# Optimization experiments

Measured on AMD Instinct MI355X. Metric: run time of the kernel, lower is better.

The kernel has to match this reference:

```python
import jax, jax.numpy as jnp
import numpy as np

INV_SQRT2 = 0.7071067811865476


def _quadrature_ops(d):
    # truncated harmonic-oscillator ladder operator: a[n, n+1] = sqrt(n+1)
    a = jnp.diag(jnp.sqrt(jnp.arange(1, d, dtype=jnp.float32)), k=1)
    X0 = (a + a.T) * INV_SQRT2
    P0 = (a - a.T) * INV_SQRT2  # real-valued stand-in for the momentum quadrature
    I = jnp.eye(d, dtype=jnp.float32)
    return I, X0, P0


def setup_inputs() -> dict:
    key = jax.random.key(0)
    ks = jax.random.split(key, 6)
    D, d, w, K = 512, 32, 8, 4
    return {
        "mps_params": jax.random.normal(ks[0], (D, d, D), dtype=jnp.float32),
        "theta": jax.random.normal(ks[1], (1,), dtype=jnp.float32),
        "env_L": jax.random.normal(ks[2], (K, D, w, D), dtype=jnp.float32) * 0.1,
        "env_R": jax.random.normal(ks[3], (K, D, w, D), dtype=jnp.float32) * 0.1,
        "coeffs": jax.random.normal(ks[4], (K, w, w, 5), dtype=jnp.float32),
        "prefactors": jax.random.normal(ks[5], (K,), dtype=jnp.float32),
    }


def reference(mps_params, theta, env_L, env_R, coeffs, prefactors):
    A = mps_params  # [D(left), d(phys), D(right)]
    d = A.shape[1]
    K = prefactors.shape[0]

    # norm_fn: psi.H @ psi for a single-tensor MPS is sum(A^2)
    An = A / jnp.sqrt(jnp.sum(A * A))

    # _get_XandP: quadrature rotation from basis params
    I, X0, P0 = _quadrature_ops(d)
    c, s = jnp.cos(theta[0]), jnp.sin(theta[0])
    X = c * X0 + s * P0
    P = -s * X0 + c * P0

    # dynamic MPO cores: W_k[i,j] = sum_c coeffs[k,i,j,c] * ops[c]
    ops = jnp.stack([I, X, P, X @ X, P @ P])  # [5, d, d]
    W = jnp.einsum('kijc,cab->kijab', coeffs, ops)  # [K, w, w, d, d]

    out = jnp.zeros((), dtype=A.dtype)
    for k in range(K):  # fixed small loop over Hamiltonian constituents
        # T: [L, w, p, r]
        T = jnp.einsum('Lwl,lpr->Lwpr', env_L[k], An)
        # apply MPO core: [L, v, P, r]
        T = jnp.einsum('wvPp,Lwpr->LvPr', W[k], T)
        # close with right env: [L, P, R]
        T = jnp.einsum('LvPr,Rvr->LPR', T, env_R[k])
        out = out + prefactors[k] * jnp.einsum('LPR,LPR->', An, T)
    return out
```

## Files before the change

kernel.cpp:

```cpp
#include <hip/hip_runtime.h>


typedef __attribute__((ext_vector_type(8))) _Float16 f16x8;
typedef __attribute__((ext_vector_type(4))) float f32x4;

#define EPS 136

__device__ __forceinline__ unsigned short f2h(float f) {
    _Float16 h = (_Float16)f;
    return *(unsigned short*)&h;
}

__device__ __forceinline__ void gload16(const void* g, void* l) {
    __builtin_amdgcn_global_load_lds(
        (const __attribute__((address_space(1))) void*)g,
        (__attribute__((address_space(3))) void*)l, 16, 0, 0);
}

struct GArg {
    const unsigned short* A;
    const unsigned short* B;
    unsigned short* C;
    int kshift;
    long long kextra;
};

__global__ __launch_bounds__(256) void gemm_dual(int K, GArg g0, GArg g1)
{
    __shared__ short sh[8704];
    const GArg g = blockIdx.z ? g1 : g0;
    const int tid = threadIdx.x;
    const int wid = tid >> 6, lane = tid & 63;

    const int flat = blockIdx.y * 128 + blockIdx.x;
    const int xcd = flat & 7;
    const int local = flat >> 3;
    const int col0 = (xcd * 16 + (local & 15)) * 128;
    const int row0 = (local >> 4) * 128;

    const int wr = (wid >> 1) * 64, wc = (wid & 1) * 64;
    const int lrow = lane & 15, kb = (lane >> 4) * 8;

    const int c0 = tid, c1 = tid + 256;
    const int r0 = c0 >> 2, kc0 = (c0 & 3) * 8;
    const int r1 = c1 >> 2, kc1 = (c1 & 3) * 8;
    const int gr0 = row0 + r0, gr1 = row0 + r1;
    const size_t aoff0 = (size_t)gr0 * 512 + (size_t)((unsigned)gr0 >> g.kshift) * g.kextra;
    const size_t aoff1 = (size_t)gr1 * 512 + (size_t)((unsigned)gr1 >> g.kshift) * g.kextra;
    const size_t boff0 = (size_t)(col0 + r0) * 512;
    const size_t boff1 = (size_t)(col0 + r1) * 512;

    f32x4 acc[4][4] = {};

    for (int k0 = 0; k0 < K; k0 += 32) {
        gload16(g.A + aoff0 + k0 + kc0, sh + c0 * 8);
        gload16(g.A + aoff1 + k0 + kc1, sh + c1 * 8);
        gload16(g.B + boff0 + k0 + kc0, sh + 4096 + c0 * 8);
        gload16(g.B + boff1 + k0 + kc1, sh + 4096 + c1 * 8);
        __syncthreads();
        f16x8 a[4], b[4];
        #pragma unroll
        for (int i = 0; i < 4; ++i)
            a[i] = *(const f16x8*)&sh[(wr + i * 16 + lrow) * 32 + kb];
        #pragma unroll
        for (int j = 0; j < 4; ++j)
            b[j] = *(const f16x8*)&sh[4096 + (wc + j * 16 + lrow) * 32 + kb];
        #pragma unroll
        for (int i = 0; i < 4; ++i)
            #pragma unroll
            for (int j = 0; j < 4; ++j)
                acc[i][j] = __builtin_amdgcn_mfma_f32_16x16x32_f16(a[i], b[j], acc[i][j], 0, 0, 0);
        __syncthreads();
    }

    const int orow = (lane >> 4) * 4, ocol = lane & 15;
    #pragma unroll
    for (int h = 0; h < 2; ++h) {
        if ((wid >> 1) == h) {
            #pragma unroll
            for (int i = 0; i < 4; ++i)
                #pragma unroll
                for (int j = 0; j < 4; ++j)
                    #pragma unroll
                    for (int q = 0; q < 4; ++q)
                        sh[(i * 16 + orow + q) * EPS + wc + j * 16 + ocol] =
                            (short)f2h(acc[i][j][q]);
        }
        __syncthreads();
        #pragma unroll
        for (int s2 = 0; s2 < 4; ++s2) {
            int idx = tid + s2 * 256;
            int rr2 = idx >> 4, ch = idx & 15;
            *(int4*)(g.C + (size_t)(row0 + h * 64 + rr2) * 16384 + col0 + ch * 8) =
                *(const int4*)(sh + rr2 * EPS + ch * 8);
        }
        __syncthreads();
    }
}

__global__ __launch_bounds__(1024) void gemm_g4w(
    const unsigned short* __restrict__ T1, const unsigned short* __restrict__ Yp,
    const float* __restrict__ W2p, float* __restrict__ dacc,
    int Lt8, int zkShift, int BKC)
{
    __shared__ short sh[16384];
    const int tid = threadIdx.x;
    const int wid = tid >> 6, lane = tid & 63;
    const int kidx = blockIdx.x >> zkShift;
    const int kz = (blockIdx.x - (kidx << zkShift)) * BKC;
    const int wr = (wid >> 2) * 64, wc = (wid & 3) * 64;
    const int lrow = lane & 15, kb = (lane >> 4) * 8;

    const int r = tid >> 2, kc = (tid & 3) * 8;
    const int w_ = r >> 5, p_ = r & 31;
    const size_t T1k = (size_t)kidx * Lt8 * 16384;
    const size_t Yk = (size_t)kidx * 4096;
    const size_t aoff = T1k + (size_t)w_ * 16384 + (size_t)p_ * 512;
    const size_t boff = Yk + (size_t)p_ * 16384 + (size_t)w_ * 512;

    f32x4 acc[4][4] = {};

    for (int k0 = 0; k0 < BKC; k0 += 32) {
        const int kk = kz + k0;
        const int lt = kk >> 9, rbase = kk & 511;
        gload16(T1 + aoff + (size_t)lt * 131072 + rbase + kc, sh + tid * 8);
        gload16(Yp + boff + (size_t)lt * 524288 + rbase + kc, sh + 8192 + tid * 8);
        __syncthreads();
        f16x8 a[4], b[4];
        #pragma unroll
        for (int i = 0; i < 4; ++i)
            a[i] = *(const f16x8*)&sh[(wr + i * 16 + lrow) * 32 + kb];
        #pragma unroll
        for (int j = 0; j < 4; ++j)
            b[j] = *(const f16x8*)&sh[8192 + (wc + j * 16 + lrow) * 32 + kb];
        #pragma unroll
        for (int i = 0; i < 4; ++i)
            #pragma unroll
            for (int j = 0; j < 4; ++j)
                acc[i][j] = __builtin_amdgcn_mfma_f32_16x16x32_f16(a[i], b[j], acc[i][j], 0, 0, 0);
        __syncthreads();
    }

    const int orow = (lane >> 4) * 4, ocol = lane & 15;
    const float* Wk = W2p + ((size_t)kidx << 16);
    float s = 0.f;
    #pragma unroll
    for (int j = 0; j < 4; ++j) {
        const int n = wc + j * 16 + ocol;
        const float* wrow = Wk + (size_t)n * 256 + wr + orow;
        #pragma unroll
        for (int i = 0; i < 4; ++i) {
            float4 wv = *(const float4*)(wrow + i * 16);
            s += wv.x * acc[i][j][0] + wv.y * acc[i][j][1]
               + wv.z * acc[i][j][2] + wv.w * acc[i][j][3];
        }
    }
    __syncthreads();
    float* red = (float*)sh;
    red[tid] = s;
    __syncthreads();
    for (int st = 512; st > 0; st >>= 1) {
        if (tid < st) red[tid] += red[tid + st];
        __syncthreads();
    }
    if (tid == 0) atomicAdd(dacc, red[0]);
}

__global__ __launch_bounds__(256) void cast_sumsq(
    const float* __restrict__ in, unsigned short* __restrict__ out,
    long long n4, float* __restrict__ sumsq)
{
    float p = 0.f;
    for (long long i = (long long)blockIdx.x * blockDim.x + threadIdx.x; i < n4;
         i += (long long)gridDim.x * blockDim.x) {
        float4 v = ((const float4*)in)[i];
        p += v.x * v.x + v.y * v.y + v.z * v.z + v.w * v.w;
        union { unsigned short s[4]; uint2 d; } o;
        o.s[0] = f2h(v.x); o.s[1] = f2h(v.y); o.s[2] = f2h(v.z); o.s[3] = f2h(v.w);
        ((uint2*)out)[i] = o.d;
    }
    __shared__ float sh[256];
    sh[threadIdx.x] = p;
    __syncthreads();
    for (int s = 128; s > 0; s >>= 1) {
        if (threadIdx.x < s) sh[threadIdx.x] += sh[threadIdx.x + s];
        __syncthreads();
    }
    if (threadIdx.x == 0) atomicAdd(sumsq, sh[0]);
}

__global__ void cast_kernel(const float* __restrict__ in, unsigned short* __restrict__ out,
                            long long n4)
{
    for (long long i = (long long)blockIdx.x * blockDim.x + threadIdx.x; i < n4;
         i += (long long)gridDim.x * blockDim.x) {
        float4 v = ((const float4*)in)[i];
        union { unsigned short s[4]; uint2 d; } o;
        o.s[0] = f2h(v.x); o.s[1] = f2h(v.y); o.s[2] = f2h(v.z); o.s[3] = f2h(v.w);
        ((uint2*)out)[i] = o.d;
    }
}

__global__ void transpose_cast(const float* __restrict__ in, unsigned short* __restrict__ out,
                               int R, int C, long long in_stride, long long out_stride)
{
    __shared__ float tile[32][33];
    in += (long long)blockIdx.z * in_stride;
    out += (long long)blockIdx.z * out_stride;
    int c0 = blockIdx.x * 32, r0 = blockIdx.y * 32;
    int tx = threadIdx.x, ty = threadIdx.y;
    #pragma unroll
    for (int i = 0; i < 4; ++i)
        tile[ty + i * 8][tx] = in[(size_t)(r0 + ty + i * 8) * C + c0 + tx];
    __syncthreads();
    #pragma unroll
    for (int i = 0; i < 4; ++i)
        out[(size_t)(c0 + ty + i * 8) * R + r0 + tx] = f2h(tile[tx][ty + i * 8]);
}

__global__ void build_ops(const float* __restrict__ theta, float* __restrict__ ops)
{
    __shared__ float X[32][32], Pm[32][32];
    int i = threadIdx.y, j = threadIdx.x;
    float c = cosf(theta[0]), s = sinf(theta[0]);
    float aij = (j == i + 1) ? sqrtf((float)j) : 0.f;
    float aji = (i == j + 1) ? sqrtf((float)i) : 0.f;
    const float inv = 0.70710678118654752440f;
    float x0 = (aij + aji) * inv;
    float p0 = (aij - aji) * inv;
    X[i][j] = c * x0 + s * p0;
    Pm[i][j] = -s * x0 + c * p0;
    __syncthreads();
    float xx = 0.f, pp = 0.f;
    #pragma unroll
    for (int m = 0; m < 32; ++m) {
        xx += X[i][m] * X[m][j];
        pp += Pm[i][m] * Pm[m][j];
    }
    ops[0 * 1024 + i * 32 + j] = (i == j) ? 1.f : 0.f;
    ops[1 * 1024 + i * 32 + j] = X[i][j];
    ops[2 * 1024 + i * 32 + j] = Pm[i][j];
    ops[3 * 1024 + i * 32 + j] = xx;
    ops[4 * 1024 + i * 32 + j] = pp;
}

__global__ void build_w(const float* __restrict__ coeffs, const float* __restrict__ ops,
                        const float* __restrict__ pref, float* __restrict__ W2)
{
    int b = blockIdx.x;
    int k = b >> 6, w = (b >> 3) & 7, v = b & 7;
    int P = threadIdx.y, p = threadIdx.x;
    const float* cf = coeffs + ((k * 8 + w) * 8 + v) * 5;
    float acc = 0.f;
    #pragma unroll
    for (int c = 0; c < 5; ++c) acc += cf[c] * ops[c * 1024 + P * 32 + p];
    W2[(size_t)k * 65536 + (v * 32 + P) * 256 + (w * 32 + p)] = acc * pref[k];
}

__global__ void finalize_kernel(const float* __restrict__ dacc, const float* __restrict__ sumsq,
                                float* __restrict__ out)
{
    if (threadIdx.x == 0) out[0] = dacc[0] / sumsq[0];
}

extern "C" void kernel_launch(void* const* d_in, const int* in_sizes, int n_in,
                              void* d_out, int out_size, void* d_ws, size_t ws_size,
                              hipStream_t stream)
{
    const float* A      = (const float*)d_in[0];
    const float* theta  = (const float*)d_in[1];
    const float* envL   = (const float*)d_in[2];
    const float* envR   = (const float*)d_in[3];
    const float* coeffs = (const float*)d_in[4];
    const float* pref   = (const float*)d_in[5];
    float* out = (float*)d_out;

    char* ws = (char*)d_ws;
    float* sumsq = (float*)ws;
    float* dacc  = (float*)(ws + 4);
    float* ops   = (float*)(ws + 64);
    float* W2    = (float*)(ws + (32 << 10));
    unsigned short* envLh  = (unsigned short*)(ws + (4ull << 20));
    unsigned short* Ah     = (unsigned short*)(ws + (21ull << 20));
    unsigned short* Ath    = (unsigned short*)(ws + (38ull << 20));
    unsigned short* envRth = (unsigned short*)(ws + (55ull << 20));
    const size_t big0 = 72ull << 20;

    int Lt = 64;
    while (Lt > 8) {
        size_t need = big0 + 2ull * (size_t)Lt * (1ull << 20);
        if (need <= ws_size) break;
        Lt >>= 1;
    }
    unsigned short* T1 = (unsigned short*)(ws + big0);
    unsigned short* Yp = T1 + (size_t)Lt * 524288;

    const int Lt8 = Lt * 8;
    const int kshiftA = __builtin_ctz(Lt8);
    const long long kextraA = 2097152LL - (long long)Lt8 * 512;
    const int KT = Lt * 512;
    int BKC = KT / 64; if (BKC < 128) BKC = 128;
    const int zk = KT / BKC;
    const int zkShift = __builtin_ctz(zk);

    hipMemsetAsync(ws, 0, 64, stream);

    cast_sumsq<<<1024, 256, 0, stream>>>(A, Ah, 2097152LL, sumsq);
    build_ops<<<1, dim3(32, 32), 0, stream>>>(theta, ops);
    build_w<<<256, dim3(32, 32), 0, stream>>>(coeffs, ops, pref, W2);
    cast_kernel<<<2048, 256, 0, stream>>>(envL, envLh, 2097152LL);
    transpose_cast<<<dim3(512, 16, 1), dim3(32, 8), 0, stream>>>(A, Ath, 512, 16384, 0, 0);
    transpose_cast<<<dim3(128, 16, 4), dim3(32, 8), 0, stream>>>(envR, envRth, 512, 4096,
                                                                 2097152LL, 2097152LL);

    const int ntiles = 512 / Lt;
    for (int t = 0; t < ntiles; ++t) {
        GArg g0, g1;
        g0.A = envLh + (size_t)t * Lt8 * 512; g0.B = Ath; g0.C = T1;
        g0.kshift = kshiftA; g0.kextra = kextraA;
        g1.A = Ah + (size_t)t * Lt * 16384; g1.B = envRth; g1.C = Yp;
        g1.kshift = 30; g1.kextra = 0;
        gemm_dual<<<dim3(128, (Lt * 32) / 128, 2), 256, 0, stream>>>(512, g0, g1);
        gemm_g4w<<<dim3(4 * zk), 1024, 0, stream>>>(T1, Yp, W2, dacc, Lt8, zkShift, BKC);
    }
    finalize_kernel<<<1, 64, 0, stream>>>(dacc, sumsq, out);
}
```

Baseline: 1.206 ms.

## Rewrite dual GEMM as 256x256 tiles with double-buffered LDS and swizzle

Replaces the 128x128, single-buffered, 256-thread dual GEMM with a 512-thread kernel computing 256x256 tiles with K-step 64. Global-to-LDS loads are double-buffered so the next tile's loads overlap MFMA work, and each thread gets more reuse per loaded fragment. It adds an XOR swizzle to avoid LDS bank conflicts and uses setprio and explicit waitcnt to schedule the waves. In exchange it uses 128KB of LDS per block, has fewer blocks per launch, and depends on hand-tuned waitcnt counts being correct.

```diff
diff --git a/kernel.cpp b/kernel.cpp
--- a/kernel.cpp
+++ b/kernel.cpp
@@ -3,8 +3,6 @@
 
 typedef __attribute__((ext_vector_type(8))) _Float16 f16x8;
 typedef __attribute__((ext_vector_type(4))) float f32x4;
-
-#define EPS 136
 
 __device__ __forceinline__ unsigned short f2h(float f) {
     _Float16 h = (_Float16)f;
@@ -25,74 +23,129 @@
     long long kextra;
 };
 
-__global__ __launch_bounds__(256) void gemm_dual(int K, GArg g0, GArg g1)
-{
-    __shared__ short sh[8704];
+__device__ __forceinline__ void stage_tile(
+    const GArg& g, int row0, int col0, int kt0,
+    short* dstA, short* dstB, int tid)
+{
+    #pragma unroll
+    for (int q = 0; q < 4; ++q) {
+        const int c = q * 512 + tid;
+        const int r = c >> 3;
+        const int gs = (c & 7) ^ (r & 7);
+        const int gr = row0 + r;
+        const size_t aoff = (size_t)gr * 512 + (size_t)((unsigned)gr >> g.kshift) * g.kextra;
+        gload16(g.A + aoff + kt0 + gs * 8, dstA + c * 8);
+        gload16(g.B + (size_t)(col0 + r) * 512 + kt0 + gs * 8, dstB + c * 8);
+    }
+}
+
+__global__ __launch_bounds__(512, 2) void gemm_dual256(int K, GArg g0, GArg g1)
+{
+    __shared__ short lds[65536];
     const GArg g = blockIdx.z ? g1 : g0;
     const int tid = threadIdx.x;
     const int wid = tid >> 6, lane = tid & 63;
-
-    const int flat = blockIdx.y * 128 + blockIdx.x;
-    const int xcd = flat & 7;
-    const int local = flat >> 3;
-    const int col0 = (xcd * 16 + (local & 15)) * 128;
-    const int row0 = (local >> 4) * 128;
-
-    const int wr = (wid >> 1) * 64, wc = (wid & 1) * 64;
-    const int lrow = lane & 15, kb = (lane >> 4) * 8;
-
-    const int c0 = tid, c1 = tid + 256;
-    const int r0 = c0 >> 2, kc0 = (c0 & 3) * 8;
-    const int r1 = c1 >> 2, kc1 = (c1 & 3) * 8;
-    const int gr0 = row0 + r0, gr1 = row0 + r1;
-    const size_t aoff0 = (size_t)gr0 * 512 + (size_t)((unsigned)gr0 >> g.kshift) * g.kextra;
-    const size_t aoff1 = (size_t)gr1 * 512 + (size_t)((unsigned)gr1 >> g.kshift) * g.kextra;
-    const size_t boff0 = (size_t)(col0 + r0) * 512;
-    const size_t boff1 = (size_t)(col0 + r1) * 512;
-
-    f32x4 acc[4][4] = {};
-
-    for (int k0 = 0; k0 < K; k0 += 32) {
-        gload16(g.A + aoff0 + k0 + kc0, sh + c0 * 8);
-        gload16(g.A + aoff1 + k0 + kc1, sh + c1 * 8);
-        gload16(g.B + boff0 + k0 + kc0, sh + 4096 + c0 * 8);
-        gload16(g.B + boff1 + k0 + kc1, sh + 4096 + c1 * 8);
-        __syncthreads();
-        f16x8 a[4], b[4];
-        #pragma unroll
-        for (int i = 0; i < 4; ++i)
-            a[i] = *(const f16x8*)&sh[(wr + i * 16 + lrow) * 32 + kb];
-        #pragma unroll
-        for (int j = 0; j < 4; ++j)
-            b[j] = *(const f16x8*)&sh[4096 + (wc + j * 16 + lrow) * 32 + kb];
+    const int wm = wid >> 2, wn = wid & 3;
+    const int lrow = lane & 15, lgrp = lane >> 4;
+    const int sx = lrow & 7;
+    const int gsw0 = (lgrp ^ sx) * 8, gsw1 = ((lgrp + 4) ^ sx) * 8;
+
+    const int flat = blockIdx.y * 64 + blockIdx.x;
+    const int xcd = flat & 7, local = flat >> 3;
+    const int col0 = (xcd * 8 + (local & 7)) * 256;
+    const int row0 = (local >> 3) * 256;
+
+    const int nt = K >> 6;
+    short* A0 = lds;          short* B0 = lds + 16384;
+    short* A1 = lds + 32768;  short* B1 = lds + 49152;
+
+    f32x4 acc[8][4] = {};
+
+    stage_tile(g, row0, col0, 0, A0, B0, tid);
+    stage_tile(g, row0, col0, 64, A1, B1, tid);
+    asm volatile("s_waitcnt vmcnt(8)" ::: "memory");
+    __builtin_amdgcn_s_barrier();
+    __builtin_amdgcn_sched_barrier(0);
+
+    for (int t = 0; t < nt; ++t) {
+        const short* cA = (t & 1) ? A1 : A0;
+        const short* cB = (t & 1) ? B1 : B0;
+        short* wA = (t & 1) ? A1 : A0;
+        short* wB = (t & 1) ? B1 : B0;
+
+        f16x8 bfr[4][2], afr[4][2];
+        #pragma unroll
+        for (int j = 0; j < 4; ++j) {
+            const int R = wn * 64 + j * 16 + lrow;
+            bfr[j][0] = *(const f16x8*)&cB[R * 64 + gsw0];
+            bfr[j][1] = *(const f16x8*)&cB[R * 64 + gsw1];
+        }
+        #pragma unroll
+        for (int i = 0; i < 4; ++i) {
+            const int R = wm * 128 + i * 16 + lrow;
+            afr[i][0] = *(const f16x8*)&cA[R * 64 + gsw0];
+            afr[i][1] = *(const f16x8*)&cA[R * 64 + gsw1];
+        }
+        __builtin_amdgcn_s_setprio(1);
         #pragma unroll
         for (int i = 0; i < 4; ++i)
             #pragma unroll
-            for (int j = 0; j < 4; ++j)
-                acc[i][j] = __builtin_amdgcn_mfma_f32_16x16x32_f16(a[i], b[j], acc[i][j], 0, 0, 0);
-        __syncthreads();
-    }
-
-    const int orow = (lane >> 4) * 4, ocol = lane & 15;
+            for (int j = 0; j < 4; ++j) {
+                acc[i][j] = __builtin_amdgcn_mfma_f32_16x16x32_f16(afr[i][0], bfr[j][0], acc[i][j], 0, 0, 0);
+                acc[i][j] = __builtin_amdgcn_mfma_f32_16x16x32_f16(afr[i][1], bfr[j][1], acc[i][j], 0, 0, 0);
+            }
+        __builtin_amdgcn_s_setprio(0);
+        #pragma unroll
+        for (int i = 0; i < 4; ++i) {
+            const int R = wm * 128 + (i + 4) * 16 + lrow;
+            afr[i][0] = *(const f16x8*)&cA[R * 64 + gsw0];
+            afr[i][1] = *(const f16x8*)&cA[R * 64 + gsw1];
+        }
+        asm volatile("s_waitcnt lgkmcnt(0)" ::: "memory");
+        __builtin_amdgcn_sched_barrier(0);
+        __builtin_amdgcn_s_barrier();
+        __builtin_amdgcn_sched_barrier(0);
+        if (t + 2 < nt)
+            stage_tile(g, row0, col0, (t + 2) * 64, wA, wB, tid);
+        __builtin_amdgcn_s_setprio(1);
+        #pragma unroll
+        for (int i = 0; i < 4; ++i)
+            #pragma unroll
+            for (int j = 0; j < 4; ++j) {
+                acc[i + 4][j] = __builtin_amdgcn_mfma_f32_16x16x32_f16(afr[i][0], bfr[j][0], acc[i + 4][j], 0, 0, 0);
+                acc[i + 4][j] = __builtin_amdgcn_mfma_f32_16x16x32_f16(afr[i][1], bfr[j][1], acc[i + 4][j], 0, 0, 0);
+            }
+        __builtin_amdgcn_s_setprio(0);
+        if (t < nt - 1) {
+            if (t + 2 < nt) asm volatile("s_waitcnt vmcnt(8)" ::: "memory");
+            else            asm volatile("s_waitcnt vmcnt(0)" ::: "memory");
+            __builtin_amdgcn_sched_barrier(0);
+            __builtin_amdgcn_s_barrier();
+            __builtin_amdgcn_sched_barrier(0);
+        }
+    }
+
+    const int orow = lgrp * 4, ocol = lrow;
+    __syncthreads();
     #pragma unroll
     for (int h = 0; h < 2; ++h) {
-        if ((wid >> 1) == h) {
+        if (wm == h) {
             #pragma unroll
-            for (int i = 0; i < 4; ++i)
+            for (int i = 0; i < 8; ++i)
                 #pragma unroll
                 for (int j = 0; j < 4; ++j)
                     #pragma unroll
                     for (int q = 0; q < 4; ++q)
-                        sh[(i * 16 + orow + q) * EPS + wc + j * 16 + ocol] =
+                        lds[(i * 16 + orow + q) * 264 + wn * 64 + j * 16 + ocol] =
                             (short)f2h(acc[i][j][q]);
         }
         __syncthreads();
         #pragma unroll
-        for (int s2 = 0; s2 < 4; ++s2) {
-            int idx = tid + s2 * 256;
-            int rr2 = idx >> 4, ch = idx & 15;
-            *(int4*)(g.C + (size_t)(row0 + h * 64 + rr2) * 16384 + col0 + ch * 8) =
-                *(const int4*)(sh + rr2 * EPS + ch * 8);
+        for (int s2 = 0; s2 < 8; ++s2) {
+            const int ch = s2 * 512 + tid;
+            const int rr = ch >> 5, c16 = ch & 31;
+            *(int4*)(g.C + (size_t)(row0 + h * 128 + rr) * 16384 + col0 + c16 * 8) =
+                *(const int4*)&lds[rr * 264 + c16 * 8];
         }
         __syncthreads();
     }
@@ -320,7 +373,7 @@
         g0.kshift = kshiftA; g0.kextra = kextraA;
         g1.A = Ah + (size_t)t * Lt * 16384; g1.B = envRth; g1.C = Yp;
         g1.kshift = 30; g1.kextra = 0;
-        gemm_dual<<<dim3(128, (Lt * 32) / 128, 2), 256, 0, stream>>>(512, g0, g1);
+        gemm_dual256<<<dim3(64, (Lt * 32) / 256, 2), 512, 0, stream>>>(512, g0, g1);
         gemm_g4w<<<dim3(4 * zk), 1024, 0, stream>>>(T1, Yp, W2, dacc, Lt8, zkShift, BKC);
     }
     finalize_kernel<<<1, 64, 0, stream>>>(dacc, sumsq, out);
```

After: 1.042 ms. 1.16x faster.
